# Performance work log

Measured on AMD Instinct MI355X. Metric: run time of the kernel, lower is better.

Reference implementation:

```python
import jax, jax.numpy as jnp
import numpy as np
import math

N, LQ, LK = 4, 2048, 2048
H, P = 16, 64
D = H * P  # 1024
EPS = 1e-5


def setup_inputs() -> dict:
    key = jax.random.key(0)
    ks = jax.random.split(key, 5)
    s = 1.0 / math.sqrt(D)
    return {
        "query": jax.random.normal(ks[0], (N, LQ, D), dtype=jnp.float32),
        "key": jax.random.normal(ks[1], (N, LK, D), dtype=jnp.float32),
        "Wq": jax.random.normal(ks[2], (D, D), dtype=jnp.float32) * s,
        "Wk": jax.random.normal(ks[3], (D, D), dtype=jnp.float32) * s,
        "Wv": jax.random.normal(ks[4], (D, D), dtype=jnp.float32) * s,
        "gamma": jnp.ones((D,), dtype=jnp.float32),
        "beta": jnp.zeros((D,), dtype=jnp.float32),
    }


def reference(query, key, Wq, Wk, Wv, gamma, beta):
    n, lq, _ = query.shape
    lk = key.shape[1]
    # Linear projections (torch Linear: x @ W.T), reshaped into heads
    q = (query @ Wq.T).reshape(n, lq, H, P)
    k = (key @ Wk.T).reshape(n, lk, H, P)
    v = (key @ Wv.T).reshape(n, lk, H, P)
    # score: (N, Lq, Lk, H), scaled by sqrt(out_channels)=sqrt(D)
    score = jnp.einsum("nqhp,nkhp->nqkh", q, k) / math.sqrt(D)
    # causal mask: triu(ones, diagonal=1) -> masked positions set to -1e6
    causal = jnp.triu(jnp.ones((lq, lk), dtype=bool), k=1)
    score = jnp.where(causal[None, :, :, None], jnp.float32(-1000000.0), score)
    attention = jax.nn.softmax(score, axis=2)  # softmax over key dim
    res = jnp.einsum("nqkh,nkhp->nqhp", attention, v).reshape(n, lq, D)
    res = res + query
    # BatchNorm0d over flattened (N*Lq, D), training-mode batch statistics
    flat = res.reshape(-1, D)
    mean = jnp.mean(flat, axis=0)
    var = jnp.var(flat, axis=0)  # biased variance, as torch BN normalization
    flat = (flat - mean) / jnp.sqrt(var + EPS) * gamma + beta
    return flat.reshape(n, lq, D)
```

## Files before the change

kernel.cpp:

```cpp
#include <hip/hip_runtime.h>
#include <hip/hip_bf16.h>

typedef __attribute__((ext_vector_type(8))) short short8;
typedef __attribute__((ext_vector_type(4))) short short4v;
typedef __attribute__((ext_vector_type(4))) float float4v;

#define LQN 2048
#define DM 1024

#define GAS __attribute__((address_space(1)))
#define LAS __attribute__((address_space(3)))

__device__ __forceinline__ short f2bf(float f) {
  unsigned u = __builtin_bit_cast(unsigned, f);
  u += 0x7fff + ((u >> 16) & 1);
  return (short)(u >> 16);
}

__device__ __forceinline__ float4v mfma_pv(short4v a, short4v b, float4v c) {
#if defined(__HIP_DEVICE_COMPILE__)
#if __has_builtin(__builtin_amdgcn_mfma_f32_16x16x16_bf16)
  return __builtin_amdgcn_mfma_f32_16x16x16_bf16(a, b, c, 0, 0, 0);
#else
  return __builtin_amdgcn_mfma_f32_16x16x16bf16_1k(a, b, c, 0, 0, 0);
#endif
#else
  (void)a; (void)b;
  return c;
#endif
}

__global__ __launch_bounds__(256) void convert_qk(const float* __restrict__ q,
                                                  const float* __restrict__ k,
                                                  short* __restrict__ dst0)
{
  const float* src = blockIdx.y ? k : q;
  short* dst = dst0 + (size_t)blockIdx.y * 8388608;
  const size_t base = ((size_t)blockIdx.x * 256 + threadIdx.x) * 8;
  float4v a = *(const float4v*)&src[base];
  float4v b = *(const float4v*)&src[base + 4];
  short8 o8 = {f2bf(a.x), f2bf(a.y), f2bf(a.z), f2bf(a.w),
               f2bf(b.x), f2bf(b.y), f2bf(b.z), f2bf(b.w)};
  *(short8*)&dst[base] = o8;
}

__global__ __launch_bounds__(256) void convert_w(const float* __restrict__ Wq,
                                                 const float* __restrict__ Wk,
                                                 const float* __restrict__ Wv,
                                                 short* __restrict__ Wbf)
{
  const int z = blockIdx.y;
  const float* src = (z == 0) ? Wq : (z == 1) ? Wk : Wv;
  short* dst = Wbf + (size_t)z * 1048576;
  const size_t base = ((size_t)blockIdx.x * 256 + threadIdx.x) * 8;
  float4v a = *(const float4v*)&src[base];
  float4v b = *(const float4v*)&src[base + 4];
  short8 o8 = {f2bf(a.x), f2bf(a.y), f2bf(a.z), f2bf(a.w),
               f2bf(b.x), f2bf(b.y), f2bf(b.z), f2bf(b.w)};
  *(short8*)&dst[base] = o8;
}

template <bool WBF>
__global__ __launch_bounds__(256, 2) void gemm_qkv(
    const short* __restrict__ Abf, const float* __restrict__ Wq,
    const float* __restrict__ Wk, const float* __restrict__ Wv,
    const short* __restrict__ Wbf,
    short* __restrict__ Qbf, short* __restrict__ Kbf, short* __restrict__ Vt)
{
  __shared__ __align__(16) short As[2 * 4096];
  __shared__ __align__(16) short Bs[2 * 4096];

  const int z = blockIdx.z;
  const short* Ag = (z == 0) ? Abf : (Abf + 8388608);
  const float* Wg = (z == 0) ? Wq : (z == 1) ? Wk : Wv;
  const short* Wbz = WBF ? (Wbf + (size_t)z * 1048576) : nullptr;

  const int m0 = blockIdx.x * 128;
  const int n0 = blockIdx.y * 128;
  const int t = threadIdx.x;
  const int lane = t & 63;
  const int lrow = lane & 15;
  const int quad = lane >> 4;
  const int wave = t >> 6;
  const int wm = (wave & 1) * 64;
  const int wn = (wave >> 1) * 64;

  const int srow = t >> 2;
  const int scol8 = (t & 3) * 8;
  const int sldsb = (t & 192) * 8;

  float4v acc[4][4];
#pragma unroll
  for (int i = 0; i < 4; i++)
#pragma unroll
    for (int j = 0; j < 4; j++) acc[i][j] = (float4v){0.f, 0.f, 0.f, 0.f};

  for (int kk = 0; kk < 1024; kk += 64) {
    __syncthreads();
#pragma unroll
    for (int pl = 0; pl < 2; pl++) {
#pragma unroll
      for (int q = 0; q < 2; q++) {
        const int row = q * 64 + srow;
        const short* gp = &Ag[(size_t)(m0 + row) * DM + kk + pl * 32 + scol8];
        short* lp = &As[pl * 4096 + (q * 256 + (t & 192)) * 8];
        __builtin_amdgcn_global_load_lds((const GAS void*)gp, (LAS void*)lp, 16, 0, 0);
        if (WBF) {
          const short* gpb = &Wbz[(size_t)(n0 + row) * DM + kk + pl * 32 + scol8];
          short* lpb = &Bs[pl * 4096 + (q * 256 + (t & 192)) * 8];
          __builtin_amdgcn_global_load_lds((const GAS void*)gpb, (LAS void*)lpb, 16, 0, 0);
        }
      }
    }
    if (!WBF) {
#pragma unroll
      for (int p = 0; p < 4; p++) {
        const int row = p * 32 + (t >> 3);
#pragma unroll
        for (int cp = 0; cp < 2; cp++) {
          const int c4 = (t & 7) * 4;
          float4v b = *(const float4v*)&Wg[(size_t)(n0 + row) * DM + kk + cp * 32 + c4];
          short4v b16 = {f2bf(b.x), f2bf(b.y), f2bf(b.z), f2bf(b.w)};
          *(short4v*)&Bs[cp * 4096 + row * 32 + c4] = b16;
        }
      }
    }
    __syncthreads();

#pragma unroll
    for (int ko = 0; ko < 2; ko++) {
      short8 af[4], bf[4];
#pragma unroll
      for (int i = 0; i < 4; i++) {
        af[i] = *(const short8*)&As[ko * 4096 + (wm + i * 16 + lrow) * 32 + quad * 8];
        bf[i] = *(const short8*)&Bs[ko * 4096 + (wn + i * 16 + lrow) * 32 + quad * 8];
      }
#pragma unroll
      for (int i = 0; i < 4; i++)
#pragma unroll
        for (int j = 0; j < 4; j++)
          acc[i][j] = __builtin_amdgcn_mfma_f32_16x16x32_bf16(af[i], bf[j],
                                                              acc[i][j], 0, 0, 0);
    }
  }

  if (z < 2) {
    short* Og = (z == 0) ? Qbf : Kbf;
    const float sc = (z == 0) ? 0.03125f * 1.44269504f : 1.0f;
#pragma unroll
    for (int i = 0; i < 4; i++)
#pragma unroll
      for (int j = 0; j < 4; j++)
#pragma unroll
        for (int r = 0; r < 4; r++) {
          const int row = m0 + wm + i * 16 + quad * 4 + r;
          const int col = n0 + wn + j * 16 + lrow;
          Og[(size_t)row * DM + col] = f2bf(acc[i][j][r] * sc);
        }
  } else {
#pragma unroll
    for (int i = 0; i < 4; i++) {
      const int rowb = m0 + wm + i * 16 + quad * 4;
      const int batch = rowb >> 11;
      const int kpos = rowb & 2047;
#pragma unroll
      for (int j = 0; j < 4; j++) {
        const int col = n0 + wn + j * 16 + lrow;
        short4v pk = {f2bf(acc[i][j][0]), f2bf(acc[i][j][1]),
                      f2bf(acc[i][j][2]), f2bf(acc[i][j][3])};
        *(short4v*)&Vt[(size_t)batch * DM * LQN + (size_t)col * LQN + kpos] = pk;
      }
    }
  }
}

__global__ __launch_bounds__(256, 4) void flash_attn(
    const short* __restrict__ Qbf, const short* __restrict__ Kbf,
    const short* __restrict__ Vt, const float* __restrict__ query,
    float* __restrict__ res)
{
  __shared__ __align__(16) short Ks[2][4096];
  __shared__ __align__(16) short Vs[2][64 * 76];

  const int b = blockIdx.x;
  const int nh = (b & 7) | ((b >> 6) << 3);
  const int pair = (b >> 3) & 7;
  const int h = nh & 15;
  const int n = nh >> 4;
  const int t = threadIdx.x;
  const int lane = t & 63;
  const int wave = t >> 6;
  const int lrow = lane & 15;
  const int quad = lane >> 4;

  const size_t rowoff = (size_t)n * LQN;
  const size_t hcol = (size_t)h * 64;
  const size_t vtoff = (size_t)n * (size_t)DM * LQN + hcol * LQN;

  const int skey = t >> 2;
  const int sq8 = (t & 3) * 8;
  const int skq = (t & 3) * 16;
  const int ldsbase = (t & 192) * 8;

#pragma unroll
  for (int half = 0; half < 2; half++) {
    const int qt = half ? (15 - pair) : pair;
    const int qb = qt * 128;
    const int wrow = qb + wave * 32;

    short8 qf[2][2];
#pragma unroll
    for (int mt = 0; mt < 2; mt++)
#pragma unroll
      for (int dh = 0; dh < 2; dh++)
        qf[mt][dh] = *(const short8*)
            &Qbf[(rowoff + wrow + mt * 16 + lrow) * DM + hcol + dh * 32 + quad * 8];

    float4v o[2][4];
#pragma unroll
    for (int mt = 0; mt < 2; mt++)
#pragma unroll
      for (int j = 0; j < 4; j++) o[mt][j] = (float4v){0.f, 0.f, 0.f, 0.f};
    float lsum[2] = {0.f, 0.f};

    const int nkt = 2 * qt + 2;

    {
      const short* g0 = &Kbf[(rowoff + skey) * DM + hcol + sq8];
      __builtin_amdgcn_global_load_lds((const GAS void*)g0,
                                       (LAS void*)&Ks[0][ldsbase], 16, 0, 0);
      const short* g1 = &Kbf[(rowoff + skey) * DM + hcol + 32 + sq8];
      __builtin_amdgcn_global_load_lds((const GAS void*)g1,
                                       (LAS void*)&Ks[0][2048 + ldsbase], 16, 0, 0);
      const short* gv = &Vt[vtoff + (size_t)skey * LQN + skq];
      short4v v0 = *(const short4v*)(gv);
      short4v v1 = *(const short4v*)(gv + 4);
      short4v v2 = *(const short4v*)(gv + 8);
      short4v v3 = *(const short4v*)(gv + 12);
      short* l = &Vs[0][skey * 76 + skq];
      *(short4v*)(l + 0) = v0;
      *(short4v*)(l + 4) = v1;
      *(short4v*)(l + 8) = v2;
      *(short4v*)(l + 12) = v3;
    }

    for (int kt = 0; kt < nkt; kt++) {
      __syncthreads();
      const int buf = kt & 1;
      const int nbuf = buf ^ 1;
      const int kbase = kt * 64;
      const bool more = (kt + 1 < nkt);

      short4v v0, v1, v2, v3;
      if (more) {
        const int kb2 = kbase + 64;
        const short* g0 = &Kbf[(rowoff + kb2 + skey) * DM + hcol + sq8];
        __builtin_amdgcn_global_load_lds((const GAS void*)g0,
                                         (LAS void*)&Ks[nbuf][ldsbase], 16, 0, 0);
        const short* g1 = &Kbf[(rowoff + kb2 + skey) * DM + hcol + 32 + sq8];
        __builtin_amdgcn_global_load_lds((const GAS void*)g1,
                                         (LAS void*)&Ks[nbuf][2048 + ldsbase], 16, 0, 0);
        const short* gv = &Vt[vtoff + (size_t)skey * LQN + kb2 + skq];
        v0 = *(const short4v*)(gv);
        v1 = *(const short4v*)(gv + 4);
        v2 = *(const short4v*)(gv + 8);
        v3 = *(const short4v*)(gv + 12);
      }

      const int drel = wrow - kbase;
#pragma unroll
      for (int f4 = 0; f4 < 4; f4++) {
        if (f4 * 16 > drel + 31) continue;
        short8 kf0 = *(const short8*)&Ks[buf][(f4 * 16 + lrow) * 32 + quad * 8];
        short8 kf1 = *(const short8*)&Ks[buf][2048 + (f4 * 16 + lrow) * 32 + quad * 8];
        short4v vf[4];
#pragma unroll
        for (int j = 0; j < 4; j++)
          vf[j] = *(const short4v*)&Vs[buf][(j * 16 + lrow) * 76 + f4 * 16 + quad * 4];
#pragma unroll
        for (int mt = 0; mt < 2; mt++) {
          if (f4 * 16 > drel + mt * 16 + 15) continue;
          float4v z = (float4v){0.f, 0.f, 0.f, 0.f};
          z = __builtin_amdgcn_mfma_f32_16x16x32_bf16(kf0, qf[mt][0], z, 0, 0, 0);
          z = __builtin_amdgcn_mfma_f32_16x16x32_bf16(kf1, qf[mt][1], z, 0, 0, 0);
          const bool pm = (f4 * 16 + 15 > drel + mt * 16);
          const int dk = drel + mt * 16 + lrow;
          short4v pk;
          float ls = 0.f;
#pragma unroll
          for (int r = 0; r < 4; r++) {
            float p = exp2f(z[r]);
            if (pm && (f4 * 16 + quad * 4 + r > dk)) p = 0.f;
            ls += p;
            pk[r] = f2bf(p);
          }
          lsum[mt] += ls;
#pragma unroll
          for (int j = 0; j < 4; j++)
            o[mt][j] = mfma_pv(pk, vf[j], o[mt][j]);
        }
      }

      if (more) {
        short* l = &Vs[nbuf][skey * 76 + skq];
        *(short4v*)(l + 0) = v0;
        *(short4v*)(l + 4) = v1;
        *(short4v*)(l + 8) = v2;
        *(short4v*)(l + 12) = v3;
      }
    }

    float inv[2][4];
#pragma unroll
    for (int mt = 0; mt < 2; mt++) {
      float s = lsum[mt];
      s += __shfl_xor(s, 16);
      s += __shfl_xor(s, 32);
#pragma unroll
      for (int r = 0; r < 4; r++) inv[mt][r] = 1.0f / __shfl(s, quad * 4 + r);
    }

#pragma unroll
    for (int mt = 0; mt < 2; mt++)
#pragma unroll
      for (int r = 0; r < 4; r++) {
        const size_t row = rowoff + wrow + mt * 16 + quad * 4 + r;
#pragma unroll
        for (int j = 0; j < 4; j++) {
          const size_t idx = row * DM + hcol + j * 16 + lrow;
          res[idx] = o[mt][j][r] * inv[mt][r] + query[idx];
        }
      }
  }
}

__global__ __launch_bounds__(256) void bn_stats(const float* __restrict__ res,
                                                float* __restrict__ stats)
{
  const int t = threadIdx.x;
  const int b = blockIdx.x;
  float4v sum = (float4v){0.f, 0.f, 0.f, 0.f};
  float4v sq = (float4v){0.f, 0.f, 0.f, 0.f};
  for (int r = 0; r < 16; r++) {
    float4v v = *(const float4v*)&res[(size_t)(b * 16 + r) * DM + t * 4];
    sum += v;
    sq += v * v;
  }
#pragma unroll
  for (int i = 0; i < 4; i++) {
    atomicAdd(&stats[t * 4 + i], sum[i]);
    atomicAdd(&stats[1024 + t * 4 + i], sq[i]);
  }
}

__global__ __launch_bounds__(256) void bn_apply(float* __restrict__ res,
                                                const float* __restrict__ stats,
                                                const float* __restrict__ gamma,
                                                const float* __restrict__ beta)
{
  const size_t i = (size_t)blockIdx.x * 256 + threadIdx.x;
  const int c = (int)(i & 255) * 4;
  float4v v = *(const float4v*)&res[i * 4];
  float4v sm = *(const float4v*)&stats[c];
  float4v sq = *(const float4v*)&stats[1024 + c];
  float4v g = *(const float4v*)&gamma[c];
  float4v bt = *(const float4v*)&beta[c];
  float4v outv;
#pragma unroll
  for (int j = 0; j < 4; j++) {
    const float mean = sm[j] * (1.0f / 8192.0f);
    const float var = sq[j] * (1.0f / 8192.0f) - mean * mean;
    outv[j] = (v[j] - mean) * rsqrtf(var + 1e-5f) * g[j] + bt[j];
  }
  *(float4v*)&res[i * 4] = outv;
}

extern "C" void kernel_launch(void* const* d_in, const int* in_sizes, int n_in,
                              void* d_out, int out_size, void* d_ws,
                              size_t ws_size, hipStream_t stream)
{
  const float* query = (const float*)d_in[0];
  const float* key   = (const float*)d_in[1];
  const float* Wq    = (const float*)d_in[2];
  const float* Wk    = (const float*)d_in[3];
  const float* Wv    = (const float*)d_in[4];
  const float* gamma = (const float*)d_in[5];
  const float* beta  = (const float*)d_in[6];
  float* out = (float*)d_out;

  char* ws = (char*)d_ws;
  short* Qbf = (short*)(ws);
  short* Kbf = (short*)(ws + (size_t)16 * 1024 * 1024);
  short* Vt  = (short*)(ws + (size_t)32 * 1024 * 1024);
  float* stats = (float*)(ws + (size_t)48 * 1024 * 1024);
  short* Wbf = (short*)(ws + (size_t)49 * 1024 * 1024);
  const bool wbf = ws_size >= ((size_t)55 << 20);

  (void)hipMemsetAsync(stats, 0, 2048 * sizeof(float), stream);

  convert_qk<<<dim3(4096, 2), 256, 0, stream>>>(query, key, (short*)d_out);
  if (wbf) {
    convert_w<<<dim3(512, 3), 256, 0, stream>>>(Wq, Wk, Wv, Wbf);
    gemm_qkv<true><<<dim3(64, 8, 3), 256, 0, stream>>>(
        (const short*)d_out, Wq, Wk, Wv, Wbf, Qbf, Kbf, Vt);
  } else {
    gemm_qkv<false><<<dim3(64, 8, 3), 256, 0, stream>>>(
        (const short*)d_out, Wq, Wk, Wv, nullptr, Qbf, Kbf, Vt);
  }
  flash_attn<<<dim3(512), 256, 0, stream>>>(Qbf, Kbf, Vt, query, out);
  bn_stats<<<dim3(512), 256, 0, stream>>>(out, stats);
  bn_apply<<<dim3(8192), 256, 0, stream>>>(out, stats, gamma, beta);
}
```

Baseline: 345.2 us.

## Split flash attention into one q-tile per block and XCD-swizzle GEMM grid

The attention kernel no longer pairs two causal q-tiles per block. It launches 1024 blocks, one q-tile each, and orders them into slots so the long and short tiles interleave for load balance. The QKV GEMM grid is flattened to 1D and remapped so that blocks landing on the same XCD share A rows, which should improve L2 reuse. The cost is more blocks to schedule and a reload of K/V per tile, since a block no longer reuses them across its two tiles.

```diff
diff --git a/kernel.cpp b/kernel.cpp
--- a/kernel.cpp
+++ b/kernel.cpp
@@ -70,13 +70,17 @@
   __shared__ __align__(16) short As[2 * 4096];
   __shared__ __align__(16) short Bs[2 * 4096];
 
-  const int z = blockIdx.z;
+  const int b = blockIdx.x;
+  const int xcd = b & 7;
+  const int w = b >> 3;
+  const int z = w >> 6;
+  const int m0 = (((w >> 3) & 7) | (xcd << 3)) * 128;
+  const int n0 = (w & 7) * 128;
+
   const short* Ag = (z == 0) ? Abf : (Abf + 8388608);
   const float* Wg = (z == 0) ? Wq : (z == 1) ? Wk : Wv;
   const short* Wbz = WBF ? (Wbf + (size_t)z * 1048576) : nullptr;
 
-  const int m0 = blockIdx.x * 128;
-  const int n0 = blockIdx.y * 128;
   const int t = threadIdx.x;
   const int lane = t & 63;
   const int lrow = lane & 15;
@@ -87,7 +91,6 @@
 
   const int srow = t >> 2;
   const int scol8 = (t & 3) * 8;
-  const int sldsb = (t & 192) * 8;
 
   float4v acc[4][4];
 #pragma unroll
@@ -119,8 +122,8 @@
 #pragma unroll
         for (int cp = 0; cp < 2; cp++) {
           const int c4 = (t & 7) * 4;
-          float4v b = *(const float4v*)&Wg[(size_t)(n0 + row) * DM + kk + cp * 32 + c4];
-          short4v b16 = {f2bf(b.x), f2bf(b.y), f2bf(b.z), f2bf(b.w)};
+          float4v bb = *(const float4v*)&Wg[(size_t)(n0 + row) * DM + kk + cp * 32 + c4];
+          short4v b16 = {f2bf(bb.x), f2bf(bb.y), f2bf(bb.z), f2bf(bb.w)};
           *(short4v*)&Bs[cp * 4096 + row * 32 + c4] = b16;
         }
       }
@@ -183,8 +186,12 @@
   __shared__ __align__(16) short Vs[2][64 * 76];
 
   const int b = blockIdx.x;
-  const int nh = (b & 7) | ((b >> 6) << 3);
-  const int pair = (b >> 3) & 7;
+  const int slot = b >> 8;
+  const int u = b & 255;
+  const int nh = u & 63;
+  const int a = u >> 6;
+  const int qt = (slot == 0) ? a : (slot == 1) ? (15 - a)
+               : (slot == 2) ? (a + 4) : (11 - a);
   const int h = nh & 15;
   const int n = nh >> 4;
   const int t = threadIdx.x;
@@ -197,141 +204,137 @@
   const size_t hcol = (size_t)h * 64;
   const size_t vtoff = (size_t)n * (size_t)DM * LQN + hcol * LQN;
 
+  const int qb = qt * 128;
+  const int wrow = qb + wave * 32;
+
+  short8 qf[2][2];
+#pragma unroll
+  for (int mt = 0; mt < 2; mt++)
+#pragma unroll
+    for (int dh = 0; dh < 2; dh++)
+      qf[mt][dh] = *(const short8*)
+          &Qbf[(rowoff + wrow + mt * 16 + lrow) * DM + hcol + dh * 32 + quad * 8];
+
+  float4v o[2][4];
+#pragma unroll
+  for (int mt = 0; mt < 2; mt++)
+#pragma unroll
+    for (int j = 0; j < 4; j++) o[mt][j] = (float4v){0.f, 0.f, 0.f, 0.f};
+  float lsum[2] = {0.f, 0.f};
+
+  const int nkt = 2 * qt + 2;
+
   const int skey = t >> 2;
   const int sq8 = (t & 3) * 8;
   const int skq = (t & 3) * 16;
   const int ldsbase = (t & 192) * 8;
 
-#pragma unroll
-  for (int half = 0; half < 2; half++) {
-    const int qt = half ? (15 - pair) : pair;
-    const int qb = qt * 128;
-    const int wrow = qb + wave * 32;
-
-    short8 qf[2][2];
-#pragma unroll
-    for (int mt = 0; mt < 2; mt++)
-#pragma unroll
-      for (int dh = 0; dh < 2; dh++)
-        qf[mt][dh] = *(const short8*)
-            &Qbf[(rowoff + wrow + mt * 16 + lrow) * DM + hcol + dh * 32 + quad * 8];
-
-    float4v o[2][4];
-#pragma unroll
-    for (int mt = 0; mt < 2; mt++)
-#pragma unroll
-      for (int j = 0; j < 4; j++) o[mt][j] = (float4v){0.f, 0.f, 0.f, 0.f};
-    float lsum[2] = {0.f, 0.f};
-
-    const int nkt = 2 * qt + 2;
-
-    {
-      const short* g0 = &Kbf[(rowoff + skey) * DM + hcol + sq8];
+  {
+    const short* g0 = &Kbf[(rowoff + skey) * DM + hcol + sq8];
+    __builtin_amdgcn_global_load_lds((const GAS void*)g0,
+                                     (LAS void*)&Ks[0][ldsbase], 16, 0, 0);
+    const short* g1 = &Kbf[(rowoff + skey) * DM + hcol + 32 + sq8];
+    __builtin_amdgcn_global_load_lds((const GAS void*)g1,
+                                     (LAS void*)&Ks[0][2048 + ldsbase], 16, 0, 0);
+    const short* gv = &Vt[vtoff + (size_t)skey * LQN + skq];
+    short4v v0 = *(const short4v*)(gv);
+    short4v v1 = *(const short4v*)(gv + 4);
+    short4v v2 = *(const short4v*)(gv + 8);
+    short4v v3 = *(const short4v*)(gv + 12);
+    short* l = &Vs[0][skey * 76 + skq];
+    *(short4v*)(l + 0) = v0;
+    *(short4v*)(l + 4) = v1;
+    *(short4v*)(l + 8) = v2;
+    *(short4v*)(l + 12) = v3;
+  }
+
+  for (int kt = 0; kt < nkt; kt++) {
+    __syncthreads();
+    const int buf = kt & 1;
+    const int nbuf = buf ^ 1;
+    const int kbase = kt * 64;
+    const bool more = (kt + 1 < nkt);
+
+    short4v v0, v1, v2, v3;
+    if (more) {
+      const int kb2 = kbase + 64;
+      const short* g0 = &Kbf[(rowoff + kb2 + skey) * DM + hcol + sq8];
       __builtin_amdgcn_global_load_lds((const GAS void*)g0,
-                                       (LAS void*)&Ks[0][ldsbase], 16, 0, 0);
-      const short* g1 = &Kbf[(rowoff + skey) * DM + hcol + 32 + sq8];
+                                       (LAS void*)&Ks[nbuf][ldsbase], 16, 0, 0);
+      const short* g1 = &Kbf[(rowoff + kb2 + skey) * DM + hcol + 32 + sq8];
       __builtin_amdgcn_global_load_lds((const GAS void*)g1,
-                                       (LAS void*)&Ks[0][2048 + ldsbase], 16, 0, 0);
-      const short* gv = &Vt[vtoff + (size_t)skey * LQN + skq];
-      short4v v0 = *(const short4v*)(gv);
-      short4v v1 = *(const short4v*)(gv + 4);
-      short4v v2 = *(const short4v*)(gv + 8);
-      short4v v3 = *(const short4v*)(gv + 12);
-      short* l = &Vs[0][skey * 76 + skq];
+                                       (LAS void*)&Ks[nbuf][2048 + ldsbase], 16, 0, 0);
+      const short* gv = &Vt[vtoff + (size_t)skey * LQN + kb2 + skq];
+      v0 = *(const short4v*)(gv);
+      v1 = *(const short4v*)(gv + 4);
+      v2 = *(const short4v*)(gv + 8);
+      v3 = *(const short4v*)(gv + 12);
+    }
+
+    const int drel = wrow - kbase;
+#pragma unroll
+    for (int f4 = 0; f4 < 4; f4++) {
+      if (f4 * 16 > drel + 31) continue;
+      short8 kf0 = *(const short8*)&Ks[buf][(f4 * 16 + lrow) * 32 + quad * 8];
+      short8 kf1 = *(const short8*)&Ks[buf][2048 + (f4 * 16 + lrow) * 32 + quad * 8];
+      short4v vf[4];
+#pragma unroll
+      for (int j = 0; j < 4; j++)
+        vf[j] = *(const short4v*)&Vs[buf][(j * 16 + lrow) * 76 + f4 * 16 + quad * 4];
+#pragma unroll
+      for (int mt = 0; mt < 2; mt++) {
+        if (f4 * 16 > drel + mt * 16 + 15) continue;
+        float4v z = (float4v){0.f, 0.f, 0.f, 0.f};
+        z = __builtin_amdgcn_mfma_f32_16x16x32_bf16(kf0, qf[mt][0], z, 0, 0, 0);
+        z = __builtin_amdgcn_mfma_f32_16x16x32_bf16(kf1, qf[mt][1], z, 0, 0, 0);
+        const bool pm = (f4 * 16 + 15 > drel + mt * 16);
+        const int dk = drel + mt * 16 + lrow;
+        short4v pk;
+        float ls = 0.f;
+#pragma unroll
+        for (int r = 0; r < 4; r++) {
+          float p = exp2f(z[r]);
+          if (pm && (f4 * 16 + quad * 4 + r > dk)) p = 0.f;
+          ls += p;
+          pk[r] = f2bf(p);
+        }
+        lsum[mt] += ls;
+#pragma unroll
+        for (int j = 0; j < 4; j++)
+          o[mt][j] = mfma_pv(pk, vf[j], o[mt][j]);
+      }
+    }
+
+    if (more) {
+      short* l = &Vs[nbuf][skey * 76 + skq];
       *(short4v*)(l + 0) = v0;
       *(short4v*)(l + 4) = v1;
       *(short4v*)(l + 8) = v2;
       *(short4v*)(l + 12) = v3;
     }
-
-    for (int kt = 0; kt < nkt; kt++) {
-      __syncthreads();
-      const int buf = kt & 1;
-      const int nbuf = buf ^ 1;
-      const int kbase = kt * 64;
-      const bool more = (kt + 1 < nkt);
-
-      short4v v0, v1, v2, v3;
-      if (more) {
-        const int kb2 = kbase + 64;
-        const short* g0 = &Kbf[(rowoff + kb2 + skey) * DM + hcol + sq8];
-        __builtin_amdgcn_global_load_lds((const GAS void*)g0,
-                                         (LAS void*)&Ks[nbuf][ldsbase], 16, 0, 0);
-        const short* g1 = &Kbf[(rowoff + kb2 + skey) * DM + hcol + 32 + sq8];
-        __builtin_amdgcn_global_load_lds((const GAS void*)g1,
-                                         (LAS void*)&Ks[nbuf][2048 + ldsbase], 16, 0, 0);
-        const short* gv = &Vt[vtoff + (size_t)skey * LQN + kb2 + skq];
-        v0 = *(const short4v*)(gv);
-        v1 = *(const short4v*)(gv + 4);
-        v2 = *(const short4v*)(gv + 8);
-        v3 = *(const short4v*)(gv + 12);
-      }
-
-      const int drel = wrow - kbase;
-#pragma unroll
-      for (int f4 = 0; f4 < 4; f4++) {
-        if (f4 * 16 > drel + 31) continue;
-        short8 kf0 = *(const short8*)&Ks[buf][(f4 * 16 + lrow) * 32 + quad * 8];
-        short8 kf1 = *(const short8*)&Ks[buf][2048 + (f4 * 16 + lrow) * 32 + quad * 8];
-        short4v vf[4];
-#pragma unroll
-        for (int j = 0; j < 4; j++)
-          vf[j] = *(const short4v*)&Vs[buf][(j * 16 + lrow) * 76 + f4 * 16 + quad * 4];
-#pragma unroll
-        for (int mt = 0; mt < 2; mt++) {
-          if (f4 * 16 > drel + mt * 16 + 15) continue;
-          float4v z = (float4v){0.f, 0.f, 0.f, 0.f};
-          z = __builtin_amdgcn_mfma_f32_16x16x32_bf16(kf0, qf[mt][0], z, 0, 0, 0);
-          z = __builtin_amdgcn_mfma_f32_16x16x32_bf16(kf1, qf[mt][1], z, 0, 0, 0);
-          const bool pm = (f4 * 16 + 15 > drel + mt * 16);
-          const int dk = drel + mt * 16 + lrow;
-          short4v pk;
-          float ls = 0.f;
-#pragma unroll
-          for (int r = 0; r < 4; r++) {
-            float p = exp2f(z[r]);
-            if (pm && (f4 * 16 + quad * 4 + r > dk)) p = 0.f;
-            ls += p;
-            pk[r] = f2bf(p);
-          }
-          lsum[mt] += ls;
-#pragma unroll
-          for (int j = 0; j < 4; j++)
-            o[mt][j] = mfma_pv(pk, vf[j], o[mt][j]);
-        }
-      }
-
-      if (more) {
-        short* l = &Vs[nbuf][skey * 76 + skq];
-        *(short4v*)(l + 0) = v0;
-        *(short4v*)(l + 4) = v1;
-        *(short4v*)(l + 8) = v2;
-        *(short4v*)(l + 12) = v3;
-      }
-    }
-
-    float inv[2][4];
-#pragma unroll
-    for (int mt = 0; mt < 2; mt++) {
-      float s = lsum[mt];
-      s += __shfl_xor(s, 16);
-      s += __shfl_xor(s, 32);
-#pragma unroll
-      for (int r = 0; r < 4; r++) inv[mt][r] = 1.0f / __shfl(s, quad * 4 + r);
-    }
-
-#pragma unroll
-    for (int mt = 0; mt < 2; mt++)
-#pragma unroll
-      for (int r = 0; r < 4; r++) {
-        const size_t row = rowoff + wrow + mt * 16 + quad * 4 + r;
-#pragma unroll
-        for (int j = 0; j < 4; j++) {
-          const size_t idx = row * DM + hcol + j * 16 + lrow;
-          res[idx] = o[mt][j][r] * inv[mt][r] + query[idx];
-        }
-      }
-  }
+  }
+
+  float inv[2][4];
+#pragma unroll
+  for (int mt = 0; mt < 2; mt++) {
+    float s = lsum[mt];
+    s += __shfl_xor(s, 16);
+    s += __shfl_xor(s, 32);
+#pragma unroll
+    for (int r = 0; r < 4; r++) inv[mt][r] = 1.0f / __shfl(s, quad * 4 + r);
+  }
+
+#pragma unroll
+  for (int mt = 0; mt < 2; mt++)
+#pragma unroll
+    for (int r = 0; r < 4; r++) {
+      const size_t row = rowoff + wrow + mt * 16 + quad * 4 + r;
+#pragma unroll
+      for (int j = 0; j < 4; j++) {
+        const size_t idx = row * DM + hcol + j * 16 + lrow;
+        res[idx] = o[mt][j][r] * inv[mt][r] + query[idx];
+      }
+    }
 }
 
 __global__ __launch_bounds__(256) void bn_stats(const float* __restrict__ res,
@@ -401,13 +404,13 @@
   convert_qk<<<dim3(4096, 2), 256, 0, stream>>>(query, key, (short*)d_out);
   if (wbf) {
     convert_w<<<dim3(512, 3), 256, 0, stream>>>(Wq, Wk, Wv, Wbf);
-    gemm_qkv<true><<<dim3(64, 8, 3), 256, 0, stream>>>(
+    gemm_qkv<true><<<dim3(1536), 256, 0, stream>>>(
         (const short*)d_out, Wq, Wk, Wv, Wbf, Qbf, Kbf, Vt);
   } else {
-    gemm_qkv<false><<<dim3(64, 8, 3), 256, 0, stream>>>(
+    gemm_qkv<false><<<dim3(1536), 256, 0, stream>>>(
         (const short*)d_out, Wq, Wk, Wv, nullptr, Qbf, Kbf, Vt);
   }
-  flash_attn<<<dim3(512), 256, 0, stream>>>(Qbf, Kbf, Vt, query, out);
+  flash_attn<<<dim3(1024), 256, 0, stream>>>(Qbf, Kbf, Vt, query, out);
   bn_stats<<<dim3(512), 256, 0, stream>>>(out, stats);
   bn_apply<<<dim3(8192), 256, 0, stream>>>(out, stats, gamma, beta);
 }
```

Result: faster. 322.5 us (-6.6%).
